# Optimization experiments

Measured on AMD Instinct MI355X. Metric: run time of the kernel, lower is better.

## Reference

```python
import jax, jax.numpy as jnp
import numpy as np

# Static config matching init_kwargs
B, T, GX, GY, C = 2, 5, 512, 512, 64   # batch, nsweeps, grid x, grid y, PFN out channels
VOXEL = np.array([0.2, 0.2, 8.0], np.float32)
PC_RANGE = np.array([-51.2, -51.2, -5.0, 51.2, 51.2, 3.0], np.float32)
EPS = 1e-3    # BatchNorm1d eps (det3d norm_cfg default)
N = 600_000   # total points
D_IN = 9      # 4 raw feats (x,y,z,r) + 3 cluster offsets + 2 center offsets


def setup_inputs() -> dict:
    key = jax.random.key(0)
    k1, k2, k3, k4, k5, k6 = jax.random.split(key, 6)
    xy = jax.random.uniform(k1, (N, 2), minval=-51.0, maxval=51.0)
    z = jax.random.uniform(k2, (N, 1), minval=-4.5, maxval=2.5)
    inten = jax.random.uniform(k3, (N, 1))
    b = jax.random.randint(k4, (N, 1), 0, B).astype(jnp.float32)
    t = jax.random.randint(k5, (N, 1), 0, T).astype(jnp.float32)
    # points format: [batch_id, x, y, z, intensity, time]
    points = jnp.concatenate([b, xy, z, inten, t], axis=1)
    W = jax.random.normal(k6, (D_IN, C), dtype=jnp.float32) * 0.05  # PFN linear (no bias)
    gamma = jnp.ones((C,), jnp.float32)   # BN weight
    beta = jnp.zeros((C,), jnp.float32)   # BN bias
    return {"points": points, "W": W, "gamma": gamma, "beta": beta}


def _forward(points, W, gamma, beta):
    vox = jnp.asarray(VOXEL)
    pcr = jnp.asarray(PC_RANGE)
    xyz = points[:, 1:4]
    coords_f = (xyz - pcr[:3]) / vox                       # (N,3) fractional voxel coords
    valid = ((coords_f[:, 0] >= 0) & (coords_f[:, 0] < GX)
             & (coords_f[:, 1] >= 0) & (coords_f[:, 1] < GY))
    cx = jnp.clip(coords_f[:, 0].astype(jnp.int32), 0, GX - 1)
    cy = jnp.clip(coords_f[:, 1].astype(jnp.int32), 0, GY - 1)
    bid = points[:, 0].astype(jnp.int32)
    tid = points[:, -1].astype(jnp.int32)
    nseg = B * T * GY * GX
    # pillar id flattened in (batch, time, y, x) order == canvas layout
    seg = ((bid * T + tid) * GY + cy) * GX + cx
    seg = jnp.where(valid, seg, nseg)                      # invalid points -> trash bin
    total = nseg + 1
    w = valid.astype(points.dtype)
    counts = jax.ops.segment_sum(w, seg, num_segments=total)                 # (total,)
    sums = jax.ops.segment_sum(xyz * w[:, None], seg, num_segments=total)    # (total,3)
    mean = sums / jnp.maximum(counts, 1.0)[:, None]        # scatter_mean of xyz per pillar
    f_cluster = xyz - mean[seg]                            # offset from pillar centroid
    center = (jnp.stack([cx, cy], 1).astype(points.dtype) * vox[:2]
              + vox[:2] * 0.5 + pcr[:2])
    f_center = xyz[:, :2] - center                         # offset from pillar center
    feats = jnp.concatenate([points[:, 1:5], f_cluster, f_center], axis=-1)  # (N,9)
    # PFNLayer: Linear(no bias) -> BatchNorm1d (train stats over valid pts) -> ReLU
    x = feats @ W                                          # (N,C)
    nvalid = jnp.maximum(w.sum(), 1.0)
    mu = (x * w[:, None]).sum(0) / nvalid
    var = (((x - mu) ** 2) * w[:, None]).sum(0) / nvalid   # biased var (train mode)
    x = jax.nn.relu(gamma * (x - mu) * jax.lax.rsqrt(var + EPS) + beta)
    # scatter_max over pillars, then dense canvas (empty pillars = 0)
    feat_max = jax.ops.segment_max(x, seg, num_segments=total)[:nseg]        # (nseg,C)
    canvas = jnp.where(counts[:nseg, None] > 0, feat_max, 0.0)
    canvas = canvas.reshape(B, T, GY, GX, C).transpose(0, 4, 1, 2, 3)        # (B,C,T,GY,GX)
    return canvas


def reference(points, W, gamma, beta):
    return _forward(points, W, gamma, beta)
```

## Files before the change

kernel.cpp:

```cpp
#include <hip/hip_runtime.h>
#include <stdint.h>
#include <float.h>


#define GXc 512
#define GYc 512
#define Bc  2
#define Tc  5
#define Cc  64
#define NSEG (Bc * Tc * GYc * GXc)
#define SBc 2048

__device__ __forceinline__ bool point_prep(const float* __restrict__ p,
    float& x, float& y, float& z, float& inten,
    int& bid, int& tid, int& cx, int& cy, int& seg)
{
    float b0 = p[0];
    x = p[1]; y = p[2]; z = p[3]; inten = p[4];
    float tf = p[5];
    float cf0 = __fmul_rn(__fadd_rn(x, 51.2f), 5.0f);
    float cf1 = __fmul_rn(__fadd_rn(y, 51.2f), 5.0f);
    bool valid = (cf0 >= 0.0f) && (cf0 < 512.0f) && (cf1 >= 0.0f) && (cf1 < 512.0f);
    int icx = (int)cf0; icx = icx < 0 ? 0 : (icx > GXc - 1 ? GXc - 1 : icx);
    int icy = (int)cf1; icy = icy < 0 ? 0 : (icy > GYc - 1 ? GYc - 1 : icy);
    cx = icx; cy = icy;
    bid = (int)b0;
    tid = (int)tf;
    seg = ((bid * Tc + tid) * GYc + cy) * GXc + cx;
    return valid;
}

extern "C" __global__ __launch_bounds__(256)
void k_count(const float* __restrict__ pts, uint32_t* __restrict__ counts,
             uint32_t* __restrict__ ctr,
             int* __restrict__ segOf, uint32_t* __restrict__ rankOf, int n)
{
    int i = blockIdx.x * 256 + threadIdx.x;
    if (i >= n) return;
    float x, y, z, it; int bid, tid, cx, cy, seg;
    bool v = point_prep(pts + (size_t)i * 6, x, y, z, it, bid, tid, cx, cy, seg);
    segOf[i] = v ? seg : -1;
    if (!v) return;
    rankOf[i] = atomicAdd(&counts[seg], 1u);
}

extern "C" __global__ __launch_bounds__(1024)
void k_offsets(const uint32_t* __restrict__ counts, uint32_t* __restrict__ ctr,
               int* __restrict__ denseOf, uint32_t* __restrict__ offOf,
               int* __restrict__ segOfDense)
{
    int tid = threadIdx.x;
    int i = blockIdx.x * 1024 + tid;
    uint32_t cnt = (i < NSEG) ? counts[i] : 0u;
    uint32_t occ = (cnt > 0u) ? 1u : 0u;
    unsigned long long v = ((unsigned long long)occ << 32) | (unsigned long long)cnt;
    unsigned long long inc = v;
    int lane = tid & 63, wid = tid >> 6;
    #pragma unroll
    for (int d = 1; d < 64; d <<= 1) {
        unsigned long long t = __shfl_up(inc, d, 64);
        if (lane >= d) inc += t;
    }
    __shared__ unsigned long long wtot[16];
    __shared__ unsigned long long wbase[16];
    __shared__ unsigned long long gbase;
    if (lane == 63) wtot[wid] = inc;
    __syncthreads();
    if (wid == 0) {
        unsigned long long w = (lane < 16) ? wtot[lane] : 0ull;
        unsigned long long s = w;
        #pragma unroll
        for (int d = 1; d < 16; d <<= 1) {
            unsigned long long t = __shfl_up(s, d, 64);
            if (lane >= d) s += t;
        }
        if (lane < 16) wbase[lane] = s - w;
        if (lane == 15)
            gbase = atomicAdd((unsigned long long*)(ctr + 2), s);
    }
    __syncthreads();
    if (i >= NSEG) return;
    unsigned long long ex = gbase + wbase[wid] + (inc - v);
    if (occ) {
        uint32_t d = (uint32_t)(ex >> 32);
        uint32_t o = (uint32_t)ex;
        denseOf[i] = (int)d;
        offOf[i] = o;
        segOfDense[d] = i;
    } else {
        denseOf[i] = -1;
    }
}

extern "C" __global__ __launch_bounds__(256)
void k_fill(const int* __restrict__ segOf, const uint32_t* __restrict__ rankOf,
            const uint32_t* __restrict__ offOf, uint32_t* __restrict__ list, int n)
{
    int i = blockIdx.x * 256 + threadIdx.x;
    if (i >= n) return;
    int s = segOf[i];
    if (s < 0) return;
    list[offOf[s] + rankOf[i]] = (uint32_t)i;
}

extern "C" __global__ __launch_bounds__(256)
void k_pillar(const float* __restrict__ pts, const uint32_t* __restrict__ counts,
              const uint32_t* __restrict__ offOf, const int* __restrict__ segOfDense,
              const uint32_t* __restrict__ list, const float* __restrict__ W,
              const uint32_t* __restrict__ ctr,
              float2* __restrict__ compact,
              double* __restrict__ px, double* __restrict__ px2)
{
    int lane = threadIdx.x & 63;
    int sub  = threadIdx.x >> 6;
    uint32_t nP = ctr[3];
    float w0 = W[0 * Cc + lane], w1 = W[1 * Cc + lane], w2 = W[2 * Cc + lane];
    float w3 = W[3 * Cc + lane], w4 = W[4 * Cc + lane], w5 = W[5 * Cc + lane];
    float w6 = W[6 * Cc + lane], w7 = W[7 * Cc + lane], w8 = W[8 * Cc + lane];
    double ax = 0.0, ax2 = 0.0;
    for (uint32_t d = blockIdx.x * 4 + sub; d < nP; d += (uint32_t)gridDim.x * 4) {
        int seg = segOfDense[d];
        uint32_t cnt = counts[seg];
        uint32_t off = offOf[seg];
        float sx = 0.f, sy = 0.f, sz = 0.f;
        for (uint32_t p = 0; p < cnt; p++) {
            const float* P = pts + (size_t)list[off + p] * 6;
            sx += P[1]; sy += P[2]; sz += P[3];
        }
        float fc = (float)cnt;
        float m0 = sx / fc, m1 = sy / fc, m2 = sz / fc;
        int cx = seg & (GXc - 1);
        int cy = (seg >> 9) & (GYc - 1);
        float ctr0 = __fadd_rn(__fadd_rn(__fmul_rn((float)cx, 0.2f), 0.1f), -51.2f);
        float ctr1 = __fadd_rn(__fadd_rn(__fmul_rn((float)cy, 0.2f), 0.1f), -51.2f);
        float mx = -FLT_MAX, mn = FLT_MAX;
        for (uint32_t p = 0; p < cnt; p++) {
            const float* P = pts + (size_t)list[off + p] * 6;
            float x = P[1], y = P[2], z = P[3], it = P[4];
            float xc;
            xc = x * w0;
            xc = fmaf(y,  w1, xc);
            xc = fmaf(z,  w2, xc);
            xc = fmaf(it, w3, xc);
            xc = fmaf(x - m0, w4, xc);
            xc = fmaf(y - m1, w5, xc);
            xc = fmaf(z - m2, w6, xc);
            xc = fmaf(x - ctr0, w7, xc);
            xc = fmaf(y - ctr1, w8, xc);
            ax  += (double)xc;
            ax2 = fma((double)xc, (double)xc, ax2);
            mx = fmaxf(mx, xc);
            mn = fminf(mn, xc);
        }
        compact[(size_t)d * 64 + lane] = make_float2(mx, mn);
    }
    __shared__ double sred[256];
    sred[threadIdx.x] = ax;
    __syncthreads();
    if (sub == 0)
        px[(size_t)blockIdx.x * 64 + lane] =
            sred[lane] + sred[lane + 64] + sred[lane + 128] + sred[lane + 192];
    __syncthreads();
    sred[threadIdx.x] = ax2;
    __syncthreads();
    if (sub == 0)
        px2[(size_t)blockIdx.x * 64 + lane] =
            sred[lane] + sred[lane + 64] + sred[lane + 128] + sred[lane + 192];
}

extern "C" __global__ __launch_bounds__(256)
void k_finalize(const double* __restrict__ px, const double* __restrict__ px2,
                const uint32_t* __restrict__ ctr,
                const float* __restrict__ gamma, const float* __restrict__ beta,
                float* __restrict__ scale, float* __restrict__ shift)
{
    int c = threadIdx.x & 63;
    int g = threadIdx.x >> 6;
    double sx = 0.0, sx2 = 0.0;
    for (int b = g; b < SBc; b += 4) {
        sx  += px[(size_t)b * 64 + c];
        sx2 += px2[(size_t)b * 64 + c];
    }
    __shared__ double sr[256];
    sr[threadIdx.x] = sx;
    __syncthreads();
    double tsx = 0.0;
    if (g == 0) tsx = sr[c] + sr[c + 64] + sr[c + 128] + sr[c + 192];
    __syncthreads();
    sr[threadIdx.x] = sx2;
    __syncthreads();
    if (g == 0) {
        double tsx2 = sr[c] + sr[c + 64] + sr[c + 128] + sr[c + 192];
        uint32_t nvu = ctr[2];
        if (nvu < 1u) nvu = 1u;
        double nv = (double)nvu;
        double mu = tsx / nv;
        double var = tsx2 / nv - mu * mu;
        float r = (float)(1.0 / sqrt(var + 0.001));
        float sc = gamma[c] * r;
        scale[c] = sc;
        shift[c] = fmaf(-(float)mu, sc, beta[c]);
    }
}

extern "C" __global__ __launch_bounds__(256)
void k_expand(const float2* __restrict__ compact, const int* __restrict__ denseOf,
              const float* __restrict__ scale, const float* __restrict__ shift,
              float* __restrict__ out)
{
    __shared__ int sdense[128];
    __shared__ float tile[128 * 65];
    int tid = threadIdx.x;
    int s0 = blockIdx.x * 128;
    if (tid < 128) sdense[tid] = denseOf[s0 + tid];
    __syncthreads();
    int w = tid >> 6, lane = tid & 63;
    float sc = scale[lane], sh = shift[lane];
    for (int k = 0; k < 32; k++) {
        int p = w * 32 + k;
        int d = sdense[p];
        float v = 0.0f;
        if (d >= 0) {
            float2 mm = compact[(size_t)d * 64 + lane];
            float sel = (sc >= 0.0f) ? mm.x : mm.y;
            v = fmaxf(fmaf(sel, sc, sh), 0.0f);
        }
        tile[p * 65 + lane] = v;
    }
    __syncthreads();
    int gx0 = s0 & (GXc - 1);
    int gy  = (s0 >> 9) & (GYc - 1);
    int bt  = s0 >> 18;
    int t   = bt % Tc;
    int b   = bt / Tc;
    int p   = tid & 127;
    int ch  = tid >> 7;
    size_t rowbase = ((size_t)gy << 9) + gx0 + p;
    for (int cc = 0; cc < 64; cc += 2) {
        int c = cc + ch;
        size_t o = ((((size_t)b * Cc + c) * Tc + t) << 18) + rowbase;
        out[o] = tile[p * 65 + c];
    }
}

extern "C" void kernel_launch(void* const* d_in, const int* in_sizes, int n_in,
                              void* d_out, int out_size, void* d_ws, size_t ws_size,
                              hipStream_t stream)
{
    const float* pts   = (const float*)d_in[0];
    const float* W     = (const float*)d_in[1];
    const float* gamma = (const float*)d_in[2];
    const float* beta  = (const float*)d_in[3];
    int n = in_sizes[0] / 6;

    uint8_t* ws = (uint8_t*)d_ws;
    size_t npad = ((size_t)n * 4 + 255) & ~(size_t)255;
    const size_t OFF_CTR    = 0;
    const size_t OFF_COUNTS = 256;
    const size_t ZERO_END   = OFF_COUNTS + (size_t)NSEG * 4;
    const size_t OFF_PX     = ZERO_END;
    const size_t OFF_PX2    = OFF_PX  + (size_t)SBc * 64 * 8;
    const size_t OFF_SCALE  = OFF_PX2 + (size_t)SBc * 64 * 8;
    const size_t OFF_SHIFT  = OFF_SCALE + 256;
    const size_t OFF_DENSE  = OFF_SHIFT + 256;
    const size_t OFF_OFFOF  = OFF_DENSE + (size_t)NSEG * 4;
    const size_t OFF_SEGOF  = OFF_OFFOF + (size_t)NSEG * 4;
    const size_t OFF_RANK   = OFF_SEGOF + npad;
    const size_t OFF_SDENSE = OFF_RANK + npad;
    const size_t OFF_LIST   = OFF_SDENSE + npad;
    const size_t OFF_COMP   = OFF_LIST + npad;

    uint32_t* ctr     = (uint32_t*)(ws + OFF_CTR);
    uint32_t* counts  = (uint32_t*)(ws + OFF_COUNTS);
    double*   px      = (double*)(ws + OFF_PX);
    double*   px2     = (double*)(ws + OFF_PX2);
    float*    scale   = (float*)(ws + OFF_SCALE);
    float*    shift   = (float*)(ws + OFF_SHIFT);
    int*      denseOf = (int*)(ws + OFF_DENSE);
    uint32_t* offOf   = (uint32_t*)(ws + OFF_OFFOF);
    int*      segOf   = (int*)(ws + OFF_SEGOF);
    uint32_t* rankOf  = (uint32_t*)(ws + OFF_RANK);
    int*      segOfD  = (int*)(ws + OFF_SDENSE);
    uint32_t* list    = (uint32_t*)(ws + OFF_LIST);
    float2*   compact = (float2*)(ws + OFF_COMP);

    hipMemsetAsync(ws, 0, ZERO_END, stream);

    k_count   <<<(n + 255) / 256, 256, 0, stream>>>(pts, counts, ctr, segOf, rankOf, n);
    k_offsets <<<(NSEG + 1023) / 1024, 1024, 0, stream>>>(counts, ctr, denseOf,
                                                          offOf, segOfD);
    k_fill    <<<(n + 255) / 256, 256, 0, stream>>>(segOf, rankOf, offOf, list, n);
    k_pillar  <<<SBc, 256, 0, stream>>>(pts, counts, offOf, segOfD, list, W, ctr,
                                        compact, px, px2);
    k_finalize<<<1, 256, 0, stream>>>(px, px2, ctr, gamma, beta, scale, shift);
    k_expand  <<<NSEG / 128, 256, 0, stream>>>(compact, denseOf, scale, shift,
                                               (float*)d_out);
}
```

Measured before the change: 1.190 ms.

## Gather point data into pillar-sorted float4 list and fold mean offset algebraically

The fill kernel now writes each point's (x,y,z,intensity) as a float4 into a pillar-sorted list instead of writing point indices, so the pillar kernel reads contiguous data rather than doing an indirect gather into the points array. The pillar mean is removed from the per-point linear combination: weights are pre-summed, the per-pillar mean term is subtracted once from max/min, and the BN sums are corrected with closed-form expressions. This turns the two passes over each pillar into one. Segment and rank are packed into a single uint2, and count and offset are stored densely per pillar. The cost is a larger workspace and slightly different float rounding from the reassociated arithmetic.

```diff
diff --git a/kernel.cpp b/kernel.cpp
--- a/kernel.cpp
+++ b/kernel.cpp
@@ -32,22 +32,21 @@
 
 extern "C" __global__ __launch_bounds__(256)
 void k_count(const float* __restrict__ pts, uint32_t* __restrict__ counts,
-             uint32_t* __restrict__ ctr,
-             int* __restrict__ segOf, uint32_t* __restrict__ rankOf, int n)
+             uint2* __restrict__ srArr, int n)
 {
     int i = blockIdx.x * 256 + threadIdx.x;
     if (i >= n) return;
     float x, y, z, it; int bid, tid, cx, cy, seg;
     bool v = point_prep(pts + (size_t)i * 6, x, y, z, it, bid, tid, cx, cy, seg);
-    segOf[i] = v ? seg : -1;
-    if (!v) return;
-    rankOf[i] = atomicAdd(&counts[seg], 1u);
+    if (!v) { srArr[i] = make_uint2(0xFFFFFFFFu, 0u); return; }
+    uint32_t r = atomicAdd(&counts[seg], 1u);
+    srArr[i] = make_uint2((uint32_t)seg, r);
 }
 
 extern "C" __global__ __launch_bounds__(1024)
 void k_offsets(const uint32_t* __restrict__ counts, uint32_t* __restrict__ ctr,
                int* __restrict__ denseOf, uint32_t* __restrict__ offOf,
-               int* __restrict__ segOfDense)
+               int* __restrict__ segOfDense, uint2* __restrict__ cntoff)
 {
     int tid = threadIdx.x;
     int i = blockIdx.x * 1024 + tid;
@@ -87,28 +86,28 @@
         denseOf[i] = (int)d;
         offOf[i] = o;
         segOfDense[d] = i;
+        cntoff[d] = make_uint2(o, cnt);
     } else {
         denseOf[i] = -1;
     }
 }
 
 extern "C" __global__ __launch_bounds__(256)
-void k_fill(const int* __restrict__ segOf, const uint32_t* __restrict__ rankOf,
-            const uint32_t* __restrict__ offOf, uint32_t* __restrict__ list, int n)
+void k_fill(const float* __restrict__ pts, const uint2* __restrict__ srArr,
+            const uint32_t* __restrict__ offOf, float4* __restrict__ list4, int n)
 {
     int i = blockIdx.x * 256 + threadIdx.x;
     if (i >= n) return;
-    int s = segOf[i];
-    if (s < 0) return;
-    list[offOf[s] + rankOf[i]] = (uint32_t)i;
-}
-
-extern "C" __global__ __launch_bounds__(256)
-void k_pillar(const float* __restrict__ pts, const uint32_t* __restrict__ counts,
-              const uint32_t* __restrict__ offOf, const int* __restrict__ segOfDense,
-              const uint32_t* __restrict__ list, const float* __restrict__ W,
-              const uint32_t* __restrict__ ctr,
-              float2* __restrict__ compact,
+    uint2 sr = srArr[i];
+    if (sr.x == 0xFFFFFFFFu) return;
+    const float* P = pts + (size_t)i * 6;
+    list4[offOf[sr.x] + sr.y] = make_float4(P[1], P[2], P[3], P[4]);
+}
+
+extern "C" __global__ __launch_bounds__(256)
+void k_pillar(const float4* __restrict__ list4, const uint2* __restrict__ cntoff,
+              const int* __restrict__ segOfDense, const float* __restrict__ W,
+              const uint32_t* __restrict__ ctr, float2* __restrict__ compact,
               double* __restrict__ px, double* __restrict__ px2)
 {
     int lane = threadIdx.x & 63;
@@ -117,42 +116,39 @@
     float w0 = W[0 * Cc + lane], w1 = W[1 * Cc + lane], w2 = W[2 * Cc + lane];
     float w3 = W[3 * Cc + lane], w4 = W[4 * Cc + lane], w5 = W[5 * Cc + lane];
     float w6 = W[6 * Cc + lane], w7 = W[7 * Cc + lane], w8 = W[8 * Cc + lane];
+    float wx = w0 + w4 + w7, wy = w1 + w5 + w8, wz = w2 + w6;
     double ax = 0.0, ax2 = 0.0;
     for (uint32_t d = blockIdx.x * 4 + sub; d < nP; d += (uint32_t)gridDim.x * 4) {
         int seg = segOfDense[d];
-        uint32_t cnt = counts[seg];
-        uint32_t off = offOf[seg];
-        float sx = 0.f, sy = 0.f, sz = 0.f;
-        for (uint32_t p = 0; p < cnt; p++) {
-            const float* P = pts + (size_t)list[off + p] * 6;
-            sx += P[1]; sy += P[2]; sz += P[3];
-        }
-        float fc = (float)cnt;
-        float m0 = sx / fc, m1 = sy / fc, m2 = sz / fc;
+        uint2 co = cntoff[d];
+        uint32_t off = co.x, cnt = co.y;
         int cx = seg & (GXc - 1);
         int cy = (seg >> 9) & (GYc - 1);
         float ctr0 = __fadd_rn(__fadd_rn(__fmul_rn((float)cx, 0.2f), 0.1f), -51.2f);
         float ctr1 = __fadd_rn(__fadd_rn(__fmul_rn((float)cy, 0.2f), 0.1f), -51.2f);
+        float cconst = -(ctr0 * w7 + ctr1 * w8);
+        float sx = 0.f, sy = 0.f, sz = 0.f;
         float mx = -FLT_MAX, mn = FLT_MAX;
+        double spb = 0.0, spb2 = 0.0;
         for (uint32_t p = 0; p < cnt; p++) {
-            const float* P = pts + (size_t)list[off + p] * 6;
-            float x = P[1], y = P[2], z = P[3], it = P[4];
-            float xc;
-            xc = x * w0;
-            xc = fmaf(y,  w1, xc);
-            xc = fmaf(z,  w2, xc);
-            xc = fmaf(it, w3, xc);
-            xc = fmaf(x - m0, w4, xc);
-            xc = fmaf(y - m1, w5, xc);
-            xc = fmaf(z - m2, w6, xc);
-            xc = fmaf(x - ctr0, w7, xc);
-            xc = fmaf(y - ctr1, w8, xc);
-            ax  += (double)xc;
-            ax2 = fma((double)xc, (double)xc, ax2);
-            mx = fmaxf(mx, xc);
-            mn = fminf(mn, xc);
+            float4 P = list4[off + p];
+            sx += P.x; sy += P.y; sz += P.z;
+            float pb = fmaf(P.x, wx,
+                       fmaf(P.y, wy,
+                       fmaf(P.z, wz,
+                       fmaf(P.w, w3, cconst))));
+            mx = fmaxf(mx, pb);
+            mn = fminf(mn, pb);
+            spb += (double)pb;
+            spb2 = fma((double)pb, (double)pb, spb2);
         }
-        compact[(size_t)d * 64 + lane] = make_float2(mx, mn);
+        float fc = (float)cnt;
+        float m0 = sx / fc, m1 = sy / fc, m2 = sz / fc;
+        float md = fmaf(m0, w4, fmaf(m1, w5, m2 * w6));
+        compact[(size_t)d * 64 + lane] = make_float2(mx - md, mn - md);
+        double mdd = (double)md, cd = (double)cnt;
+        ax  += spb - cd * mdd;
+        ax2 += spb2 - 2.0 * mdd * spb + cd * mdd * mdd;
     }
     __shared__ double sred[256];
     sred[threadIdx.x] = ax;
@@ -264,11 +260,11 @@
     const size_t OFF_SHIFT  = OFF_SCALE + 256;
     const size_t OFF_DENSE  = OFF_SHIFT + 256;
     const size_t OFF_OFFOF  = OFF_DENSE + (size_t)NSEG * 4;
-    const size_t OFF_SEGOF  = OFF_OFFOF + (size_t)NSEG * 4;
-    const size_t OFF_RANK   = OFF_SEGOF + npad;
-    const size_t OFF_SDENSE = OFF_RANK + npad;
-    const size_t OFF_LIST   = OFF_SDENSE + npad;
-    const size_t OFF_COMP   = OFF_LIST + npad;
+    const size_t OFF_SDENSE = OFF_OFFOF + (size_t)NSEG * 4;
+    const size_t OFF_CNTOFF = OFF_SDENSE + (size_t)NSEG * 4;
+    const size_t OFF_SR     = OFF_CNTOFF + (size_t)NSEG * 8;
+    const size_t OFF_LIST   = OFF_SR + npad * 2;
+    const size_t OFF_COMP   = OFF_LIST + npad * 4;
 
     uint32_t* ctr     = (uint32_t*)(ws + OFF_CTR);
     uint32_t* counts  = (uint32_t*)(ws + OFF_COUNTS);
@@ -278,19 +274,19 @@
     float*    shift   = (float*)(ws + OFF_SHIFT);
     int*      denseOf = (int*)(ws + OFF_DENSE);
     uint32_t* offOf   = (uint32_t*)(ws + OFF_OFFOF);
-    int*      segOf   = (int*)(ws + OFF_SEGOF);
-    uint32_t* rankOf  = (uint32_t*)(ws + OFF_RANK);
     int*      segOfD  = (int*)(ws + OFF_SDENSE);
-    uint32_t* list    = (uint32_t*)(ws + OFF_LIST);
+    uint2*    cntoff  = (uint2*)(ws + OFF_CNTOFF);
+    uint2*    srArr   = (uint2*)(ws + OFF_SR);
+    float4*   list4   = (float4*)(ws + OFF_LIST);
     float2*   compact = (float2*)(ws + OFF_COMP);
 
     hipMemsetAsync(ws, 0, ZERO_END, stream);
 
-    k_count   <<<(n + 255) / 256, 256, 0, stream>>>(pts, counts, ctr, segOf, rankOf, n);
+    k_count   <<<(n + 255) / 256, 256, 0, stream>>>(pts, counts, srArr, n);
     k_offsets <<<(NSEG + 1023) / 1024, 1024, 0, stream>>>(counts, ctr, denseOf,
-                                                          offOf, segOfD);
-    k_fill    <<<(n + 255) / 256, 256, 0, stream>>>(segOf, rankOf, offOf, list, n);
-    k_pillar  <<<SBc, 256, 0, stream>>>(pts, counts, offOf, segOfD, list, W, ctr,
+                                                          offOf, segOfD, cntoff);
+    k_fill    <<<(n + 255) / 256, 256, 0, stream>>>(pts, srArr, offOf, list4, n);
+    k_pillar  <<<SBc, 256, 0, stream>>>(list4, cntoff, segOfD, W, ctr,
                                         compact, px, px2);
     k_finalize<<<1, 256, 0, stream>>>(px, px2, ctr, gamma, beta, scale, shift);
     k_expand  <<<NSEG / 128, 256, 0, stream>>>(compact, denseOf, scale, shift,
```

Result: faster. 1.152 ms (-3.2%).
